# Kernel tuning notes

Hardware: AMD Instinct MI355X
Metric: run time of the kernel (lower is better)

Reference implementation:

```python
import jax, jax.numpy as jnp
import numpy as np

N_HEAD = 12


def setup_inputs() -> dict:
    key = jax.random.key(0)
    ks = jax.random.split(key, 5)
    B, T, C = 2, 2048, 768
    x = jax.random.normal(ks[0], (B, T, C), dtype=jnp.float32)
    w_attn = jax.random.normal(ks[1], (3 * C, C), dtype=jnp.float32) * 0.02
    b_attn = jax.random.normal(ks[2], (3 * C,), dtype=jnp.float32) * 0.02
    w_proj = jax.random.normal(ks[3], (C, C), dtype=jnp.float32) * 0.02
    b_proj = jax.random.normal(ks[4], (C,), dtype=jnp.float32) * 0.02
    return {"x": x, "w_attn": w_attn, "b_attn": b_attn, "w_proj": w_proj, "b_proj": b_proj}


def reference(x, w_attn, b_attn, w_proj, b_proj):
    B, T, C = x.shape
    H = N_HEAD
    D = C // H
    # fused QKV projection (torch Linear: x @ W.T + b)
    qkv = x @ w_attn.T + b_attn                      # [B, T, 3C]
    q, k, v = jnp.split(qkv, 3, axis=-1)
    q = q.reshape(B, T, H, D).transpose(0, 2, 1, 3)  # [B, H, T, D]
    k = k.reshape(B, T, H, D).transpose(0, 2, 1, 3)
    v = v.reshape(B, T, H, D).transpose(0, 2, 1, 3)
    # NOTE: original scales by 1/sqrt(k.size(0)) == 1/sqrt(B) (batch!), reproduced faithfully
    scale = 1.0 / jnp.sqrt(jnp.asarray(B, dtype=x.dtype))
    scores = jnp.einsum("bhtd,bhsd->bhts", q, k) * scale  # [B, H, T, T]
    causal = jnp.tril(jnp.ones((T, T), dtype=bool))
    scores = jnp.where(causal[None, None], scores, jnp.asarray(-jnp.inf, dtype=x.dtype))
    attn = jax.nn.softmax(scores, axis=-1)
    # dropout layers are identity in eval mode
    out = jnp.einsum("bhts,bhsd->bhtd", attn, v)     # [B, H, T, D]
    out = out.transpose(0, 2, 1, 3).reshape(B, T, C)
    return out @ w_proj.T + b_proj
```

## Files before the change

### kernel.cpp

```cpp
#include <hip/hip_runtime.h>
#include <hip/hip_bf16.h>
#include <stdint.h>

typedef __bf16 bf16;
typedef __bf16 bf16x4 __attribute__((ext_vector_type(4)));
typedef __bf16 bf16x8 __attribute__((ext_vector_type(8)));
typedef float f32x4 __attribute__((ext_vector_type(4)));

__device__ __forceinline__ f32x4 mfma16(bf16x8 a, bf16x8 b, f32x4 c) {
    return __builtin_amdgcn_mfma_f32_16x16x32_bf16(a, b, c, 0, 0, 0);
}

__device__ __forceinline__ void gload_lds16(const void* g, void* l) {
    __builtin_amdgcn_global_load_lds((__attribute__((address_space(1))) void*)g,
                                     (__attribute__((address_space(3))) void*)l,
                                     16, 0, 0);
}

__global__ void k_cast3(const float* __restrict__ x, const float* __restrict__ wa,
                        const float* __restrict__ wp, bf16* __restrict__ xb,
                        bf16* __restrict__ wab, bf16* __restrict__ wpb) {
    const int N1 = 786432, N2 = 442368, N3 = 147456;
    int i = blockIdx.x * blockDim.x + threadIdx.x;
    int stride = gridDim.x * blockDim.x;
    for (; i < N1 + N2 + N3; i += stride) {
        const float* src; bf16* dst; int j = i;
        if (j < N1)           { src = x;  dst = xb; }
        else if (j < N1 + N2) { src = wa; dst = wab; j -= N1; }
        else                  { src = wp; dst = wpb; j -= N1 + N2; }
        float4 v = reinterpret_cast<const float4*>(src)[j];
        bf16x4 o = { (bf16)v.x, (bf16)v.y, (bf16)v.z, (bf16)v.w };
        reinterpret_cast<bf16x4*>(dst)[j] = o;
    }
}

template<int BN, bool BF16_OUT>
__global__ __launch_bounds__(256) void k_gemm_bt(
        const bf16* __restrict__ A, const bf16* __restrict__ W,
        const float* __restrict__ bias, void* __restrict__ Cout,
        int M, int N, int K) {
    constexpr int FN = BN / 32;
    __shared__ bf16 As[128 * 64];
    __shared__ bf16 Ws[BN * 64];
    const int tid = threadIdx.x;
    const int l = tid & 63, w = tid >> 6;
    const int lr = l & 15, lq = l >> 4;
    const int wm = w >> 1, wn = w & 1;

    const int nwg = gridDim.x;
    const int q8 = nwg >> 3;
    const int swz = (blockIdx.x & 7) * q8 + (blockIdx.x >> 3);
    const int nbx = N / BN;
    const int bm = (swz / nbx) * 128, bn = (swz % nbx) * BN;

    f32x4 acc[4][FN] = {};

    for (int k0 = 0; k0 < K; k0 += 64) {
        __syncthreads();
        #pragma unroll
        for (int i = 0; i < 4; ++i) {
            int c = tid + i * 256;
            int row = c >> 3, j = c & 7;
            int src8 = (j ^ (row & 7)) * 8;
            gload_lds16(A + (size_t)(bm + row) * K + k0 + src8, As + c * 8);
        }
        #pragma unroll
        for (int i = 0; i < FN; ++i) {
            int c = tid + i * 256;
            int row = c >> 3, j = c & 7;
            int src8 = (j ^ (row & 7)) * 8;
            gload_lds16(W + (size_t)(bn + row) * K + k0 + src8, Ws + c * 8);
        }
        __syncthreads();
        bf16x8 af[2][4], wf[2][FN];
        #pragma unroll
        for (int ks = 0; ks < 2; ++ks) {
            #pragma unroll
            for (int f = 0; f < 4; ++f) {
                int ra = wm * 64 + f * 16 + lr;
                af[ks][f] = *reinterpret_cast<const bf16x8*>(
                    As + ra * 64 + (((ks * 4 + lq) ^ (lr & 7)) * 8));
            }
            #pragma unroll
            for (int f = 0; f < FN; ++f) {
                int rb = wn * (FN * 16) + f * 16 + lr;
                wf[ks][f] = *reinterpret_cast<const bf16x8*>(
                    Ws + rb * 64 + (((ks * 4 + lq) ^ (lr & 7)) * 8));
            }
        }
        #pragma unroll
        for (int ks = 0; ks < 2; ++ks)
            #pragma unroll
            for (int fm = 0; fm < 4; ++fm)
                #pragma unroll
                for (int fn = 0; fn < FN; ++fn)
                    acc[fm][fn] = mfma16(af[ks][fm], wf[ks][fn], acc[fm][fn]);
    }

    #pragma unroll
    for (int fm = 0; fm < 4; ++fm) {
        #pragma unroll
        for (int fn = 0; fn < FN; ++fn) {
            int row = bm + wm * 64 + fm * 16 + lq * 4;
            int col = bn + wn * (FN * 16) + fn * 16 + lr;
            float bv = bias[col];
            #pragma unroll
            for (int r = 0; r < 4; ++r) {
                float v = acc[fm][fn][r] + bv;
                if (BF16_OUT)
                    ((bf16*)Cout)[(size_t)(row + r) * N + col] = (bf16)v;
                else
                    ((float*)Cout)[(size_t)(row + r) * N + col] = v;
            }
        }
    }
}

__global__ __launch_bounds__(256) void k_transV(const bf16* __restrict__ qkv,
                                                bf16* __restrict__ vT) {
    const int g = blockIdx.x;
    const int bh = g >> 4, tc = g & 15;
    const int h = bh % 12, b = bh / 12;
    const int t0 = tc * 128;
    __shared__ bf16 Lt[128][68];
    const bf16* src = qkv + (size_t)(b * 2048 + t0) * 2304 + 1536 + h * 64;
    const int tid = threadIdx.x;
    #pragma unroll
    for (int ii = 0; ii < 4; ++ii) {
        int tt = ii * 32 + (tid >> 3);
        int ch = tid & 7;
        bf16x8 v = *reinterpret_cast<const bf16x8*>(src + (size_t)tt * 2304 + ch * 8);
        union { bf16x8 v8; bf16x4 h4[2]; } u; u.v8 = v;
        *reinterpret_cast<bf16x4*>(&Lt[tt][ch * 8])     = u.h4[0];
        *reinterpret_cast<bf16x4*>(&Lt[tt][ch * 8 + 4]) = u.h4[1];
    }
    __syncthreads();
    bf16* dst = vT + (size_t)bh * 64 * 2048 + t0;
    const int d = tid >> 2;
    #pragma unroll
    for (int ii = 0; ii < 4; ++ii) {
        int tch = ii * 4 + (tid & 3);
        bf16x8 v;
        #pragma unroll
        for (int e = 0; e < 8; ++e) v[e] = Lt[tch * 8 + e][d];
        *reinterpret_cast<bf16x8*>(&dst[(size_t)d * 2048 + tch * 8]) = v;
    }
}

#define CLOG2E 1.02014439f

__global__ __launch_bounds__(256, 4) void k_flash_attn(
        const bf16* __restrict__ qkv, const bf16* __restrict__ vT,
        bf16* __restrict__ att, float* __restrict__ part, int mode) {
    __shared__ bf16 Ks[3][4096];
    __shared__ bf16 VTs[2][4096];

    const int tid = threadIdx.x;
    const int l = tid & 63, w = tid >> 6;
    const int lr = l & 15, lq = l >> 4;

    const int bid = blockIdx.x;
    int qb, h, b, jt0, jt1, slot;
    bool dopart;
    if (mode) {
        int bh = bid % 24, idx = bid / 24;
        h = bh % 12; b = bh / 12;
        if (idx < 16)      { qb = 16 + idx;  jt0 = 0;  jt1 = 16;     dopart = true;  slot = (bh * 16 + idx) * 2; }
        else if (idx < 32) { qb = 47 - idx;  jt0 = 16; jt1 = qb + 1; dopart = true;  slot = (bh * 16 + (qb - 16)) * 2 + 1; }
        else               { qb = 47 - idx;  jt0 = 0;  jt1 = qb + 1; dopart = false; slot = 0; }
    } else {
        const int s = bid >> 8, i = (bid >> 3) & 31, t7 = bid & 7;
        if (s == 0)      qb = i;
        else if (s == 2) qb = (i + 16) & 31;
        else             qb = (i < 8) ? (31 - 2 * i) : (i < 16) ? (30 - 2 * i)
                           : (i < 24) ? (62 - 2 * i) : (63 - 2 * i);
        const int hb = s * 8 + t7;
        h = hb % 12; b = hb / 12;
        jt0 = 0; jt1 = qb + 1; dopart = false; slot = 0;
    }

    const bf16* Qp  = qkv + (size_t)b * 2048 * 2304 + h * 64;
    const bf16* Kp  = Qp + 768;
    const bf16* Vtp = vT + (size_t)(b * 12 + h) * 64 * 2048;

    const int qr0 = qb * 64 + w * 16;

    bf16x8 qf[2];
    #pragma unroll
    for (int ks = 0; ks < 2; ++ks)
        qf[ks] = *reinterpret_cast<const bf16x8*>(
            Qp + (size_t)(qr0 + lr) * 2304 + ks * 32 + lq * 8);

    f32x4 o[4] = {};
    float lsum = 0.f;

    auto stageK = [&](int buf, int kv0) {
        #pragma unroll
        for (int ii = 0; ii < 2; ++ii) {
            int c = tid + ii * 256;
            int row = c >> 3, j = c & 7;
            gload_lds16(Kp + (size_t)(kv0 + row) * 2304 + ((j ^ (row & 7)) * 8),
                        &Ks[buf][c * 8]);
        }
    };
    auto stageV = [&](int buf, int kv0) {
        #pragma unroll
        for (int ii = 0; ii < 2; ++ii) {
            int c = tid + ii * 256;
            int row = c >> 3, j = c & 7;
            gload_lds16(Vtp + (size_t)row * 2048 + kv0 + ((j ^ (row & 7)) * 8),
                        &VTs[buf][c * 8]);
        }
    };

    stageK(0, jt0 * 64);
    stageV(0, jt0 * 64);
    const bool two = (jt1 > jt0 + 1);
    if (two) stageK(1, jt0 * 64 + 64);
    if (two) asm volatile("s_waitcnt vmcnt(2)" ::: "memory");
    else     asm volatile("s_waitcnt vmcnt(0)" ::: "memory");
    __builtin_amdgcn_s_barrier();
    asm volatile("" ::: "memory");

    for (int jt = jt0; jt < jt1; ++jt) {
        const int curK = (jt - jt0) % 3;
        const int curV = (jt - jt0) & 1;
        const int kv0 = jt * 64;
        if (jt + 1 < jt1) stageV(curV ^ 1, kv0 + 64);
        if (jt + 2 < jt1) stageK((jt + 2 - jt0) % 3, kv0 + 128);

        const bool diag = (jt == qb);
        const int rsw = lr & 7;
        float p[4][4];
        __builtin_amdgcn_s_setprio(1);
        #pragma unroll
        for (int t = 0; t < 4; ++t) {
            f32x4 sacc = {0.f, 0.f, 0.f, 0.f};
            #pragma unroll
            for (int ks = 0; ks < 2; ++ks) {
                bf16x8 kf = *reinterpret_cast<const bf16x8*>(
                    &Ks[curK][(t * 16 + lr) * 64 + (((ks * 4 + lq) ^ rsw) * 8)]);
                sacc = mfma16(kf, qf[ks], sacc);
            }
            #pragma unroll
            for (int r = 0; r < 4; ++r)
                p[t][r] = __builtin_amdgcn_exp2f(sacc[r] * CLOG2E);
        }
        __builtin_amdgcn_s_setprio(0);
        if (diag) {
            #pragma unroll
            for (int t = 0; t < 4; ++t)
                #pragma unroll
                for (int r = 0; r < 4; ++r)
                    if (t * 16 + lq * 4 + r > w * 16 + lr) p[t][r] = 0.f;
        }
        {
            float s0 = (p[0][0] + p[0][1]) + (p[0][2] + p[0][3]);
            float s1 = (p[1][0] + p[1][1]) + (p[1][2] + p[1][3]);
            float s2 = (p[2][0] + p[2][1]) + (p[2][2] + p[2][3]);
            float s3 = (p[3][0] + p[3][1]) + (p[3][2] + p[3][3]);
            lsum += (s0 + s1) + (s2 + s3);
        }

        unsigned P0[4], P1[4];
        #pragma unroll
        for (int t = 0; t < 4; ++t) {
            asm("v_cvt_pk_bf16_f32 %0, %1, %2" : "=v"(P0[t]) : "v"(p[t][0]), "v"(p[t][1]));
            asm("v_cvt_pk_bf16_f32 %0, %1, %2" : "=v"(P1[t]) : "v"(p[t][2]), "v"(p[t][3]));
        }
        #pragma unroll
        for (int ks = 0; ks < 2; ++ks) {
            unsigned a0 = P0[2 * ks], b0 = P0[2 * ks + 1];
            asm volatile("v_permlane32_swap_b32 %0, %1" : "+v"(a0), "+v"(b0));
            asm volatile("v_permlane16_swap_b32 %0, %1" : "+v"(a0), "+v"(b0));
            unsigned a1 = P1[2 * ks], b1 = P1[2 * ks + 1];
            asm volatile("v_permlane32_swap_b32 %0, %1" : "+v"(a1), "+v"(b1));
            asm volatile("v_permlane16_swap_b32 %0, %1" : "+v"(a1), "+v"(b1));
            union { unsigned u[4]; bf16x8 v8; } pk_;
            pk_.u[0] = a0; pk_.u[1] = a1; pk_.u[2] = b0; pk_.u[3] = b1;
            bf16x8 pa = pk_.v8;
            __builtin_amdgcn_s_setprio(1);
            #pragma unroll
            for (int db = 0; db < 4; ++db) {
                bf16x8 vf = *reinterpret_cast<const bf16x8*>(
                    &VTs[curV][(db * 16 + lr) * 64 + (((ks * 4 + lq) ^ rsw) * 8)]);
                o[db] = mfma16(pa, vf, o[db]);
            }
            __builtin_amdgcn_s_setprio(0);
        }

        if (jt + 1 < jt1) {
            if (jt + 2 < jt1) asm volatile("s_waitcnt vmcnt(2)" ::: "memory");
            else              asm volatile("s_waitcnt vmcnt(0)" ::: "memory");
        }
        __builtin_amdgcn_s_barrier();
        asm volatile("" ::: "memory");
    }

    lsum += __shfl_xor(lsum, 16);
    lsum += __shfl_xor(lsum, 32);

    if (dopart) {
        float* pb = part + (size_t)slot * 4160;
        #pragma unroll
        for (int db = 0; db < 4; ++db)
            #pragma unroll
            for (int r = 0; r < 4; ++r)
                pb[(w * 16 + lq * 4 + r) * 64 + db * 16 + lr] = o[db][r];
        if (lq == 0) pb[4096 + w * 16 + lr] = lsum;
    } else {
        float inv[4];
        #pragma unroll
        for (int r = 0; r < 4; ++r)
            inv[r] = 1.0f / __shfl(lsum, lq * 4 + r);
        #pragma unroll
        for (int db = 0; db < 4; ++db)
            #pragma unroll
            for (int r = 0; r < 4; ++r) {
                float v = o[db][r] * inv[r];
                att[(size_t)(b * 2048 + qr0 + lq * 4 + r) * 768 + h * 64 + db * 16 + lr] = (bf16)v;
            }
    }
}

__global__ __launch_bounds__(256) void k_attn_reduce(
        const float* __restrict__ part, bf16* __restrict__ att) {
    int g = blockIdx.x;
    int bh = g / 16, q16 = g % 16, qb = 16 + q16;
    int h = bh % 12, b = bh / 12;
    const float* p0 = part + (size_t)((bh * 16 + q16) * 2) * 4160;
    const float* p1 = p0 + 4160;
    for (int e = threadIdx.x; e < 4096; e += 256) {
        int row = e >> 6, col = e & 63;
        float O = p0[e] + p1[e];
        float L = p0[4096 + row] + p1[4096 + row];
        att[(size_t)(b * 2048 + qb * 64 + row) * 768 + h * 64 + col] = (bf16)(O / L);
    }
}

extern "C" void kernel_launch(void* const* d_in, const int* in_sizes, int n_in,
                              void* d_out, int out_size, void* d_ws, size_t ws_size,
                              hipStream_t stream) {
    const float* x      = (const float*)d_in[0];
    const float* w_attn = (const float*)d_in[1];
    const float* b_attn = (const float*)d_in[2];
    const float* w_proj = (const float*)d_in[3];
    const float* b_proj = (const float*)d_in[4];

    char* ws = (char*)d_ws;
    bf16* xb   = (bf16*)(ws + 0);
    bf16* vT   = (bf16*)(ws + 0);
    bf16* wab  = (bf16*)(ws + 6291456);
    bf16* wpb  = (bf16*)(ws + 9830400);
    bf16* qkv  = (bf16*)(ws + 11010048);
    bf16* att  = (bf16*)(ws + 29884416);
    float* part = (float*)(ws + 36175872);
    const unsigned long long WS_NEEDED = 36175872ull + 12779520ull;

    k_cast3<<<2048, 256, 0, stream>>>(x, w_attn, w_proj, xb, wab, wpb);

    k_gemm_bt<128, true><<<576, 256, 0, stream>>>(xb, wab, b_attn, qkv, 4096, 2304, 768);

    k_transV<<<384, 256, 0, stream>>>(qkv, vT);

    if (ws_size >= WS_NEEDED) {
        k_flash_attn<<<1152, 256, 0, stream>>>(qkv, vT, att, part, 1);
        k_attn_reduce<<<384, 256, 0, stream>>>(part, att);
    } else {
        k_flash_attn<<<768, 256, 0, stream>>>(qkv, vT, att, part, 0);
    }

    k_gemm_bt<64, false><<<384, 256, 0, stream>>>(att, wpb, b_proj, d_out, 4096, 768, 768);
}
```

Measured before the change: 85.58 us.

## Split attention waves 2x2 over query and key halves to reuse LDS fragments

Reassigns the four waves so each handles 32 query rows against half of the 64-key tile, reusing each K and V LDS fragment for two MFMAs. This halves LDS fragment reads per MFMA in the inner loop. The partial outputs and row sums of the two key halves are then combined through shared memory with an extra barrier before the final store. This raises register pressure and adds an epilogue reduction.

```diff
diff --git a/kernel.cpp b/kernel.cpp
--- a/kernel.cpp
+++ b/kernel.cpp
@@ -158,6 +158,7 @@
     const int tid = threadIdx.x;
     const int l = tid & 63, w = tid >> 6;
     const int lr = l & 15, lq = l >> 4;
+    const int qh = w >> 1, hv = w & 1;
 
     const int bid = blockIdx.x;
     int qb, h, b, jt0, jt1, slot;
@@ -183,16 +184,16 @@
     const bf16* Kp  = Qp + 768;
     const bf16* Vtp = vT + (size_t)(b * 12 + h) * 64 * 2048;
 
-    const int qr0 = qb * 64 + w * 16;
-
-    bf16x8 qf[2];
+    bf16x8 qf[2][2];
     #pragma unroll
-    for (int ks = 0; ks < 2; ++ks)
-        qf[ks] = *reinterpret_cast<const bf16x8*>(
-            Qp + (size_t)(qr0 + lr) * 2304 + ks * 32 + lq * 8);
-
-    f32x4 o[4] = {};
-    float lsum = 0.f;
+    for (int qg = 0; qg < 2; ++qg)
+        #pragma unroll
+        for (int ks = 0; ks < 2; ++ks)
+            qf[qg][ks] = *reinterpret_cast<const bf16x8*>(
+                Qp + (size_t)(qb * 64 + qh * 32 + qg * 16 + lr) * 2304 + ks * 32 + lq * 8);
+
+    f32x4 o[2][4] = {};
+    float lsum0 = 0.f, lsum1 = 0.f;
 
     auto stageK = [&](int buf, int kv0) {
         #pragma unroll
@@ -222,6 +223,8 @@
     __builtin_amdgcn_s_barrier();
     asm volatile("" ::: "memory");
 
+    const int rsw = lr & 7;
+
     for (int jt = jt0; jt < jt1; ++jt) {
         const int curK = (jt - jt0) % 3;
         const int curV = (jt - jt0) & 1;
@@ -230,64 +233,72 @@
         if (jt + 2 < jt1) stageK((jt + 2 - jt0) % 3, kv0 + 128);
 
         const bool diag = (jt == qb);
-        const int rsw = lr & 7;
-        float p[4][4];
+        float p[2][2][4];
         __builtin_amdgcn_s_setprio(1);
         #pragma unroll
-        for (int t = 0; t < 4; ++t) {
-            f32x4 sacc = {0.f, 0.f, 0.f, 0.f};
-            #pragma unroll
-            for (int ks = 0; ks < 2; ++ks) {
-                bf16x8 kf = *reinterpret_cast<const bf16x8*>(
-                    &Ks[curK][(t * 16 + lr) * 64 + (((ks * 4 + lq) ^ rsw) * 8)]);
-                sacc = mfma16(kf, qf[ks], sacc);
+        for (int tp = 0; tp < 2; ++tp) {
+            const int row = hv * 32 + tp * 16 + lr;
+            bf16x8 kf0 = *reinterpret_cast<const bf16x8*>(
+                &Ks[curK][row * 64 + ((lq ^ rsw) * 8)]);
+            bf16x8 kf1 = *reinterpret_cast<const bf16x8*>(
+                &Ks[curK][row * 64 + (((4 + lq) ^ rsw) * 8)]);
+            #pragma unroll
+            for (int qg = 0; qg < 2; ++qg) {
+                f32x4 s = {0.f, 0.f, 0.f, 0.f};
+                s = mfma16(kf0, qf[qg][0], s);
+                s = mfma16(kf1, qf[qg][1], s);
+                #pragma unroll
+                for (int r = 0; r < 4; ++r)
+                    p[tp][qg][r] = __builtin_amdgcn_exp2f(s[r] * CLOG2E);
             }
-            #pragma unroll
-            for (int r = 0; r < 4; ++r)
-                p[t][r] = __builtin_amdgcn_exp2f(sacc[r] * CLOG2E);
         }
         __builtin_amdgcn_s_setprio(0);
         if (diag) {
             #pragma unroll
-            for (int t = 0; t < 4; ++t)
-                #pragma unroll
-                for (int r = 0; r < 4; ++r)
-                    if (t * 16 + lq * 4 + r > w * 16 + lr) p[t][r] = 0.f;
+            for (int tp = 0; tp < 2; ++tp)
+                #pragma unroll
+                for (int qg = 0; qg < 2; ++qg)
+                    #pragma unroll
+                    for (int r = 0; r < 4; ++r)
+                        if (hv * 32 + tp * 16 + lq * 4 + r > qh * 32 + qg * 16 + lr)
+                            p[tp][qg][r] = 0.f;
         }
         {
-            float s0 = (p[0][0] + p[0][1]) + (p[0][2] + p[0][3]);
-            float s1 = (p[1][0] + p[1][1]) + (p[1][2] + p[1][3]);
-            float s2 = (p[2][0] + p[2][1]) + (p[2][2] + p[2][3]);
-            float s3 = (p[3][0] + p[3][1]) + (p[3][2] + p[3][3]);
-            lsum += (s0 + s1) + (s2 + s3);
-        }
-
-        unsigned P0[4], P1[4];
-        #pragma unroll
-        for (int t = 0; t < 4; ++t) {
-            asm("v_cvt_pk_bf16_f32 %0, %1, %2" : "=v"(P0[t]) : "v"(p[t][0]), "v"(p[t][1]));
-            asm("v_cvt_pk_bf16_f32 %0, %1, %2" : "=v"(P1[t]) : "v"(p[t][2]), "v"(p[t][3]));
-        }
-        #pragma unroll
-        for (int ks = 0; ks < 2; ++ks) {
-            unsigned a0 = P0[2 * ks], b0 = P0[2 * ks + 1];
-            asm volatile("v_permlane32_swap_b32 %0, %1" : "+v"(a0), "+v"(b0));
-            asm volatile("v_permlane16_swap_b32 %0, %1" : "+v"(a0), "+v"(b0));
-            unsigned a1 = P1[2 * ks], b1 = P1[2 * ks + 1];
-            asm volatile("v_permlane32_swap_b32 %0, %1" : "+v"(a1), "+v"(b1));
-            asm volatile("v_permlane16_swap_b32 %0, %1" : "+v"(a1), "+v"(b1));
+            float a0 = (p[0][0][0] + p[0][0][1]) + (p[0][0][2] + p[0][0][3]);
+            float a1 = (p[1][0][0] + p[1][0][1]) + (p[1][0][2] + p[1][0][3]);
+            lsum0 += a0 + a1;
+            float b0 = (p[0][1][0] + p[0][1][1]) + (p[0][1][2] + p[0][1][3]);
+            float b1 = (p[1][1][0] + p[1][1][1]) + (p[1][1][2] + p[1][1][3]);
+            lsum1 += b0 + b1;
+        }
+
+        bf16x8 pa[2];
+        #pragma unroll
+        for (int qg = 0; qg < 2; ++qg) {
+            unsigned A0, B0, A1, B1;
+            asm("v_cvt_pk_bf16_f32 %0, %1, %2" : "=v"(A0) : "v"(p[0][qg][0]), "v"(p[0][qg][1]));
+            asm("v_cvt_pk_bf16_f32 %0, %1, %2" : "=v"(A1) : "v"(p[0][qg][2]), "v"(p[0][qg][3]));
+            asm("v_cvt_pk_bf16_f32 %0, %1, %2" : "=v"(B0) : "v"(p[1][qg][0]), "v"(p[1][qg][1]));
+            asm("v_cvt_pk_bf16_f32 %0, %1, %2" : "=v"(B1) : "v"(p[1][qg][2]), "v"(p[1][qg][3]));
+            asm volatile("v_permlane32_swap_b32 %0, %1" : "+v"(A0), "+v"(B0));
+            asm volatile("v_permlane16_swap_b32 %0, %1" : "+v"(A0), "+v"(B0));
+            asm volatile("v_permlane32_swap_b32 %0, %1" : "+v"(A1), "+v"(B1));
+            asm volatile("v_permlane16_swap_b32 %0, %1" : "+v"(A1), "+v"(B1));
             union { unsigned u[4]; bf16x8 v8; } pk_;
-            pk_.u[0] = a0; pk_.u[1] = a1; pk_.u[2] = b0; pk_.u[3] = b1;
-            bf16x8 pa = pk_.v8;
-            __builtin_amdgcn_s_setprio(1);
-            #pragma unroll
-            for (int db = 0; db < 4; ++db) {
-                bf16x8 vf = *reinterpret_cast<const bf16x8*>(
-                    &VTs[curV][(db * 16 + lr) * 64 + (((ks * 4 + lq) ^ rsw) * 8)]);
-                o[db] = mfma16(pa, vf, o[db]);
-            }
-            __builtin_amdgcn_s_setprio(0);
-        }
+            pk_.u[0] = A0; pk_.u[1] = A1; pk_.u[2] = B0; pk_.u[3] = B1;
+            pa[qg] = pk_.v8;
+        }
+
+        __builtin_amdgcn_s_setprio(1);
+        #pragma unroll
+        for (int db = 0; db < 4; ++db) {
+            const int row = db * 16 + lr;
+            bf16x8 vf = *reinterpret_cast<const bf16x8*>(
+                &VTs[curV][row * 64 + (((hv * 4 + lq) ^ rsw) * 8)]);
+            o[0][db] = mfma16(pa[0], vf, o[0][db]);
+            o[1][db] = mfma16(pa[1], vf, o[1][db]);
+        }
+        __builtin_amdgcn_s_setprio(0);
 
         if (jt + 1 < jt1) {
             if (jt + 2 < jt1) asm volatile("s_waitcnt vmcnt(2)" ::: "memory");
@@ -297,29 +308,66 @@
         asm volatile("" ::: "memory");
     }
 
-    lsum += __shfl_xor(lsum, 16);
-    lsum += __shfl_xor(lsum, 32);
-
-    if (dopart) {
-        float* pb = part + (size_t)slot * 4160;
-        #pragma unroll
-        for (int db = 0; db < 4; ++db)
-            #pragma unroll
-            for (int r = 0; r < 4; ++r)
-                pb[(w * 16 + lq * 4 + r) * 64 + db * 16 + lr] = o[db][r];
-        if (lq == 0) pb[4096 + w * 16 + lr] = lsum;
-    } else {
-        float inv[4];
-        #pragma unroll
-        for (int r = 0; r < 4; ++r)
-            inv[r] = 1.0f / __shfl(lsum, lq * 4 + r);
-        #pragma unroll
-        for (int db = 0; db < 4; ++db)
-            #pragma unroll
-            for (int r = 0; r < 4; ++r) {
-                float v = o[db][r] * inv[r];
-                att[(size_t)(b * 2048 + qr0 + lq * 4 + r) * 768 + h * 64 + db * 16 + lr] = (bf16)v;
+    lsum0 += __shfl_xor(lsum0, 16); lsum0 += __shfl_xor(lsum0, 32);
+    lsum1 += __shfl_xor(lsum1, 16); lsum1 += __shfl_xor(lsum1, 32);
+
+    {
+        float* xf = (float*)&Ks[0][0];
+        float* rg = xf + (size_t)(qh * 64 + l) * 34;
+        if (hv == 1) {
+            #pragma unroll
+            for (int qg = 0; qg < 2; ++qg)
+                #pragma unroll
+                for (int db = 0; db < 4; ++db)
+                    #pragma unroll
+                    for (int r = 0; r < 4; ++r)
+                        rg[qg * 16 + db * 4 + r] = o[qg][db][r];
+            rg[32] = lsum0; rg[33] = lsum1;
+        }
+        __syncthreads();
+        if (hv == 0) {
+            #pragma unroll
+            for (int qg = 0; qg < 2; ++qg)
+                #pragma unroll
+                for (int db = 0; db < 4; ++db)
+                    #pragma unroll
+                    for (int r = 0; r < 4; ++r)
+                        o[qg][db][r] += rg[qg * 16 + db * 4 + r];
+            lsum0 += rg[32]; lsum1 += rg[33];
+
+            if (dopart) {
+                float* pb = part + (size_t)slot * 4160;
+                #pragma unroll
+                for (int qg = 0; qg < 2; ++qg) {
+                    #pragma unroll
+                    for (int db = 0; db < 4; ++db)
+                        #pragma unroll
+                        for (int r = 0; r < 4; ++r)
+                            pb[(qh * 32 + qg * 16 + lq * 4 + r) * 64 + db * 16 + lr] = o[qg][db][r];
+                }
+                if (lq == 0) {
+                    pb[4096 + qh * 32 + lr]      = lsum0;
+                    pb[4096 + qh * 32 + 16 + lr] = lsum1;
+                }
+            } else {
+                float inv0[4], inv1[4];
+                #pragma unroll
+                for (int r = 0; r < 4; ++r) {
+                    inv0[r] = 1.0f / __shfl(lsum0, lq * 4 + r);
+                    inv1[r] = 1.0f / __shfl(lsum1, lq * 4 + r);
+                }
+                #pragma unroll
+                for (int db = 0; db < 4; ++db)
+                    #pragma unroll
+                    for (int r = 0; r < 4; ++r) {
+                        int q0 = qb * 64 + qh * 32 + lq * 4 + r;
+                        att[(size_t)(b * 2048 + q0) * 768 + h * 64 + db * 16 + lr] =
+                            (bf16)(o[0][db][r] * inv0[r]);
+                        att[(size_t)(b * 2048 + q0 + 16) * 768 + h * 64 + db * 16 + lr] =
+                            (bf16)(o[1][db][r] * inv1[r]);
+                    }
             }
+        }
     }
 }
 
```

Result: no change. 84.97 us, median of 4 (-0.7%).
